# Optimization experiments

Hardware: AMD Instinct MI355X
Metric: run time of the kernel (lower is better)

Reference implementation:

```python
import jax, jax.numpy as jnp
import numpy as np

N_DIMS, N_EMBD, N_LAYER = 64, 256, 12
B, N = 32, 1024
LN_EPS = 1e-5


def setup_inputs() -> dict:
    key = jax.random.key(0)
    ks = jax.random.split(key, 16)
    s = 0.02
    inp = {
        'xs': jax.random.normal(ks[0], (B, N, N_DIMS - 1), dtype=jnp.float32),
        'ys': jax.random.normal(ks[1], (B, N), dtype=jnp.float32),
        # read-in linear
        'W_in': jax.random.normal(ks[2], (N_DIMS, N_EMBD), dtype=jnp.float32) * s,
        'b_in': jnp.zeros((N_EMBD,), jnp.float32),
        # per-layer attention projections (no bias)
        'Wq': jax.random.normal(ks[3], (N_LAYER, N_EMBD, N_EMBD), dtype=jnp.float32) * s,
        'Wk': jax.random.normal(ks[4], (N_LAYER, N_EMBD, N_EMBD), dtype=jnp.float32) * s,
        'Wv': jax.random.normal(ks[5], (N_LAYER, N_EMBD, N_EMBD), dtype=jnp.float32) * s,
        # layernorm 1
        'g1': jnp.ones((N_LAYER, N_EMBD), jnp.float32),
        'be1': jnp.zeros((N_LAYER, N_EMBD), jnp.float32),
        # mlp: Linear -> ReLU -> Linear
        'W1': jax.random.normal(ks[6], (N_LAYER, N_EMBD, N_EMBD), dtype=jnp.float32) * s,
        'b1': jnp.zeros((N_LAYER, N_EMBD), jnp.float32),
        'W2': jax.random.normal(ks[7], (N_LAYER, N_EMBD, N_EMBD), dtype=jnp.float32) * s,
        'b2': jnp.zeros((N_LAYER, N_EMBD), jnp.float32),
        # layernorm 2
        'g2': jnp.ones((N_LAYER, N_EMBD), jnp.float32),
        'be2': jnp.zeros((N_LAYER, N_EMBD), jnp.float32),
        # read-out linear
        'W_out': jax.random.normal(ks[8], (N_EMBD, 1), dtype=jnp.float32) * s,
        'b_out': jnp.zeros((1,), jnp.float32),
    }
    return inp


def _layernorm(x, g, b):
    mu = jnp.mean(x, axis=-1, keepdims=True)
    var = jnp.mean(jnp.square(x - mu), axis=-1, keepdims=True)
    return (x - mu) * jax.lax.rsqrt(var + LN_EPS) * g + b


def reference(xs, ys, W_in, b_in, Wq, Wk, Wv, g1, be1, W1, b1, W2, b2, g2, be2, W_out, b_out):
    n = ys.shape[1]
    # _combine: zs [B, N, d+1], zero the y slot of the last (test) token
    zs = jnp.concatenate([xs, ys[:, :, None]], axis=2)
    zs = zs.at[:, -1, -1].set(0.0)
    H = zs @ W_in + b_in  # [B, N, E]
    for i in range(N_LAYER):
        q = H @ Wq[i]
        k = H @ Wk[i]
        v = H @ Wv[i]
        attn = jax.nn.relu(jnp.einsum('bid,bjd->bij', q, k)) / n
        H = H + jnp.einsum('bij,bjd->bid', attn, v)
        H = _layernorm(H, g1[i], be1[i])
        H = H + (jax.nn.relu(H @ W1[i] + b1[i]) @ W2[i] + b2[i])
        H = _layernorm(H, g2[i], be2[i])
    pred = H @ W_out + b_out  # [B, N, 1]
    return pred[:, :n, 0]  # default inds = arange(ys.shape[1])
```

## Files before the change

kernel.cpp:

```cpp
#include <hip/hip_runtime.h>
#include <math.h>

#define E 256
#define NTOK 1024
#define NB 32
#define NLAYER 12
#define LN_EPS 1e-5f

typedef __attribute__((ext_vector_type(8))) short bf16x8;
typedef __attribute__((ext_vector_type(4))) float f32x4;
#define MFMA16(a, b, c) __builtin_amdgcn_mfma_f32_16x16x32_bf16(a, b, c, 0, 0, 0)

__device__ __forceinline__ ushort f2bf(float f) {
    union { float f; unsigned u; } v; v.f = f;
    return (ushort)((v.u + 0x7fffu + ((v.u >> 16) & 1u)) >> 16);
}

__global__ __launch_bounds__(256) void k_wprep(
    const float* __restrict__ Wq, const float* __restrict__ Wk, const float* __restrict__ Wv,
    const float* __restrict__ W1, const float* __restrict__ W2,
    ushort* __restrict__ WT)
{
    const int mat = blockIdx.x % 5;
    const int l   = blockIdx.x / 5;
    const float* src = (mat == 0 ? Wq : mat == 1 ? Wk : mat == 2 ? Wv : mat == 3 ? W1 : W2)
                       + (size_t)l * E * E;
    ushort* dst = WT + ((size_t)(l * 5 + mat) << 16);
    const int n = threadIdx.x;
    #pragma unroll
    for (int c = 0; c < 4; ++c) {
        #pragma unroll
        for (int j = 0; j < 8; ++j) {
            const int k0 = c * 64 + j * 8;
            uint4 u;
            u.x = (uint)f2bf(src[(size_t)(k0 + 0) * E + n]) | ((uint)f2bf(src[(size_t)(k0 + 1) * E + n]) << 16);
            u.y = (uint)f2bf(src[(size_t)(k0 + 2) * E + n]) | ((uint)f2bf(src[(size_t)(k0 + 3) * E + n]) << 16);
            u.z = (uint)f2bf(src[(size_t)(k0 + 4) * E + n]) | ((uint)f2bf(src[(size_t)(k0 + 5) * E + n]) << 16);
            u.w = (uint)f2bf(src[(size_t)(k0 + 6) * E + n]) | ((uint)f2bf(src[(size_t)(k0 + 7) * E + n]) << 16);
            *(uint4*)&dst[(size_t)n * E + k0] = u;
        }
    }
}

__global__ __launch_bounds__(256) void k_embed(
    const float* __restrict__ xs, const float* __restrict__ ys,
    const float* __restrict__ W_in, const float* __restrict__ b_in,
    float* __restrict__ H, ushort* __restrict__ Hb)
{
    __shared__ float zs[16][64];
    const int tid = threadIdx.x;
    const int r0 = blockIdx.x * 16;
    #pragma unroll
    for (int l = 0; l < 4; ++l) {
        int lin = tid + l * 256;
        int i = lin >> 6, d = lin & 63;
        int row = r0 + i;
        int t = row & (NTOK - 1);
        float v;
        if (d < 63) v = xs[(size_t)row * 63 + d];
        else        v = (t == NTOK - 1) ? 0.f : ys[row];
        zs[i][d] = v;
    }
    __syncthreads();
    float acc[16];
    #pragma unroll
    for (int i = 0; i < 16; ++i) acc[i] = 0.f;
    for (int d = 0; d < 64; ++d) {
        float w = W_in[d * E + tid];
        #pragma unroll
        for (int i = 0; i < 16; ++i) acc[i] = fmaf(zs[i][d], w, acc[i]);
    }
    float bb = b_in[tid];
    #pragma unroll
    for (int i = 0; i < 16; ++i) {
        float o = acc[i] + bb;
        H [(size_t)(r0 + i) * E + tid] = o;
        Hb[(size_t)(r0 + i) * E + tid] = f2bf(o);
    }
}

__device__ __forceinline__ void qkv_gemm(
    const ushort* __restrict__ Wt, const ushort* __restrict__ Hb,
    size_t r0, int tid, int w, int lr, int lg,
    ushort (&Ws)[256][72], f32x4 (&acc)[4][4])
{
    #pragma unroll
    for (int mt = 0; mt < 4; ++mt)
        #pragma unroll
        for (int nt = 0; nt < 4; ++nt) acc[mt][nt] = (f32x4){0.f, 0.f, 0.f, 0.f};
    #pragma unroll 1
    for (int kc = 0; kc < 4; ++kc) {
        __syncthreads();
        #pragma unroll
        for (int rep = 0; rep < 8; ++rep) {
            int lin = rep * 256 + tid;
            int n = lin >> 3, slot = lin & 7;
            bf16x8 v = *(const bf16x8*)&Wt[(size_t)n * E + kc * 64 + slot * 8];
            *(bf16x8*)&Ws[n][slot * 8] = v;
        }
        __syncthreads();
        #pragma unroll
        for (int kl = 0; kl < 2; ++kl) {
            bf16x8 af[4], bw[4];
            #pragma unroll
            for (int mt = 0; mt < 4; ++mt)
                af[mt] = *(const bf16x8*)&Hb[(r0 + mt * 16 + lr) * E + kc * 64 + kl * 32 + lg * 8];
            #pragma unroll
            for (int nt = 0; nt < 4; ++nt)
                bw[nt] = *(const bf16x8*)&Ws[w * 64 + nt * 16 + lr][kl * 32 + lg * 8];
            #pragma unroll
            for (int mt = 0; mt < 4; ++mt)
                #pragma unroll
                for (int nt = 0; nt < 4; ++nt)
                    acc[mt][nt] = MFMA16(af[mt], bw[nt], acc[mt][nt]);
        }
    }
}

__device__ __forceinline__ void qkv_out_qk(
    ushort* __restrict__ Out, size_t r0, int w, int l, int lr, int lg,
    ushort (&ScW)[16][72], f32x4 (&acc)[4][4])
{
    #pragma unroll
    for (int mt = 0; mt < 4; ++mt) {
        #pragma unroll
        for (int nt = 0; nt < 4; ++nt)
            #pragma unroll
            for (int r = 0; r < 4; ++r)
                ScW[lg * 4 + r][nt * 16 + lr] = f2bf(acc[mt][nt][r]);
        #pragma unroll
        for (int j = 0; j < 2; ++j) {
            bf16x8 v = *(const bf16x8*)&ScW[l >> 2][(l & 3) * 16 + j * 8];
            *(bf16x8*)&Out[(r0 + mt * 16 + (l >> 2)) * E + w * 64 + (l & 3) * 16 + j * 8] = v;
        }
    }
}

__global__ __launch_bounds__(256, 2) void k_qkv(
    const ushort* __restrict__ Hb,
    const ushort* __restrict__ WqT, const ushort* __restrict__ WkT, const ushort* __restrict__ WvT,
    ushort* __restrict__ Qb, ushort* __restrict__ Kb, ushort* __restrict__ VTg)
{
    __shared__ __align__(16) ushort Ws[256][72];
    __shared__ __align__(16) ushort Sc[4][16][72];
    const int tid = threadIdx.x;
    const int w = tid >> 6, l = tid & 63;
    const int lr = l & 15, lg = l >> 4;
    const size_t r0 = (size_t)blockIdx.x * 64;
    const int b    = (int)(r0 >> 10);
    const int tok0 = (int)(r0 & (NTOK - 1));

    f32x4 acc[4][4];

    qkv_gemm(WqT, Hb, r0, tid, w, lr, lg, Ws, acc);
    qkv_out_qk(Qb, r0, w, l, lr, lg, Sc[w], acc);

    qkv_gemm(WkT, Hb, r0, tid, w, lr, lg, Ws, acc);
    qkv_out_qk(Kb, r0, w, l, lr, lg, Sc[w], acc);

    qkv_gemm(WvT, Hb, r0, tid, w, lr, lg, Ws, acc);
    __syncthreads();
    #pragma unroll
    for (int mt = 0; mt < 4; ++mt)
        #pragma unroll
        for (int nt = 0; nt < 4; ++nt) {
            ushort4 u;
            u.x = f2bf(acc[mt][nt][0]); u.y = f2bf(acc[mt][nt][1]);
            u.z = f2bf(acc[mt][nt][2]); u.w = f2bf(acc[mt][nt][3]);
            *(ushort4*)&Ws[w * 64 + nt * 16 + lr][mt * 16 + lg * 4] = u;
        }
    __syncthreads();
    #pragma unroll
    for (int rep = 0; rep < 8; ++rep) {
        int lin = rep * 256 + tid;
        int row = lin >> 3, ch = lin & 7;
        bf16x8 v = *(const bf16x8*)&Ws[row][ch * 8];
        *(bf16x8*)&VTg[((size_t)b * E + row) * NTOK + tok0 + ch * 8] = v;
    }
}

__global__ __launch_bounds__(512, 2) void k_attn(
    const ushort* __restrict__ Qb, const ushort* __restrict__ Kb, const ushort* __restrict__ VTg,
    float* __restrict__ H, ushort* __restrict__ HbO,
    const float* __restrict__ g1, const float* __restrict__ be1)
{
    __shared__ __align__(16) ushort Ks[64][264];
    __shared__ __align__(16) ushort VT[256][72];
    __shared__ __align__(16) ushort Pl[8][16][72];
    const int tid = threadIdx.x;
    const int w  = tid >> 6, l = tid & 63;
    const int lr = l & 15, lg = l >> 4;

    const int bid   = blockIdx.x;
    const int batch = bid & 31;
    const int tile  = bid >> 5;

    const size_t kvbase = (size_t)batch * NTOK * E;
    const size_t vtbase = (size_t)batch * E * NTOK;
    const int    qrow0  = tile * 128 + w * 16;
    const size_t qbase  = kvbase + (size_t)qrow0 * E;

    bf16x8 qf[8];
    #pragma unroll
    for (int kk = 0; kk < 8; ++kk)
        qf[kk] = *(const bf16x8*)&Qb[qbase + (size_t)lr * E + kk * 32 + lg * 8];

    f32x4 o[16];
    #pragma unroll
    for (int nt = 0; nt < 16; ++nt) o[nt] = (f32x4){0.f, 0.f, 0.f, 0.f};

    const float inv_n = 1.0f / (float)NTOK;
    const int krow = tid >> 5, kch = tid & 31;
    const int vrow = tid >> 3, vch = tid & 7;

    bf16x8 ck0, ck1, ck2, ck3, cv0, cv1, cv2, cv3;
    {
        ck0 = *(const bf16x8*)&Kb[kvbase + (size_t)( 0 + krow) * E + kch * 8];
        ck1 = *(const bf16x8*)&Kb[kvbase + (size_t)(16 + krow) * E + kch * 8];
        ck2 = *(const bf16x8*)&Kb[kvbase + (size_t)(32 + krow) * E + kch * 8];
        ck3 = *(const bf16x8*)&Kb[kvbase + (size_t)(48 + krow) * E + kch * 8];
        cv0 = *(const bf16x8*)&VTg[vtbase + (size_t)(  0 + vrow) * NTOK + vch * 8];
        cv1 = *(const bf16x8*)&VTg[vtbase + (size_t)( 64 + vrow) * NTOK + vch * 8];
        cv2 = *(const bf16x8*)&VTg[vtbase + (size_t)(128 + vrow) * NTOK + vch * 8];
        cv3 = *(const bf16x8*)&VTg[vtbase + (size_t)(192 + vrow) * NTOK + vch * 8];
    }

    #pragma unroll 1
    for (int jt = 0; jt < 16; ++jt) {
        __syncthreads();
        *(bf16x8*)&Ks[ 0 + krow][kch * 8] = ck0;
        *(bf16x8*)&Ks[16 + krow][kch * 8] = ck1;
        *(bf16x8*)&Ks[32 + krow][kch * 8] = ck2;
        *(bf16x8*)&Ks[48 + krow][kch * 8] = ck3;
        *(bf16x8*)&VT[  0 + vrow][vch * 8] = cv0;
        *(bf16x8*)&VT[ 64 + vrow][vch * 8] = cv1;
        *(bf16x8*)&VT[128 + vrow][vch * 8] = cv2;
        *(bf16x8*)&VT[192 + vrow][vch * 8] = cv3;
        bf16x8 nk0, nk1, nk2, nk3, nv0, nv1, nv2, nv3;
        {
            const int kn = ((jt + 1) & 15) * 64;
            nk0 = *(const bf16x8*)&Kb[kvbase + (size_t)(kn +  0 + krow) * E + kch * 8];
            nk1 = *(const bf16x8*)&Kb[kvbase + (size_t)(kn + 16 + krow) * E + kch * 8];
            nk2 = *(const bf16x8*)&Kb[kvbase + (size_t)(kn + 32 + krow) * E + kch * 8];
            nk3 = *(const bf16x8*)&Kb[kvbase + (size_t)(kn + 48 + krow) * E + kch * 8];
            nv0 = *(const bf16x8*)&VTg[vtbase + (size_t)(  0 + vrow) * NTOK + kn + vch * 8];
            nv1 = *(const bf16x8*)&VTg[vtbase + (size_t)( 64 + vrow) * NTOK + kn + vch * 8];
            nv2 = *(const bf16x8*)&VTg[vtbase + (size_t)(128 + vrow) * NTOK + kn + vch * 8];
            nv3 = *(const bf16x8*)&VTg[vtbase + (size_t)(192 + vrow) * NTOK + kn + vch * 8];
        }
        __syncthreads();

        __builtin_amdgcn_s_setprio(1);
        f32x4 s0 = (f32x4){0.f, 0.f, 0.f, 0.f};
        f32x4 s1 = s0, s2 = s0, s3 = s0;
        #pragma unroll
        for (int kk = 0; kk < 8; ++kk) {
            bf16x8 b0 = *(const bf16x8*)&Ks[     lr][kk * 32 + lg * 8];
            bf16x8 b1 = *(const bf16x8*)&Ks[16 + lr][kk * 32 + lg * 8];
            bf16x8 b2 = *(const bf16x8*)&Ks[32 + lr][kk * 32 + lg * 8];
            bf16x8 b3 = *(const bf16x8*)&Ks[48 + lr][kk * 32 + lg * 8];
            s0 = MFMA16(qf[kk], b0, s0);
            s1 = MFMA16(qf[kk], b1, s1);
            s2 = MFMA16(qf[kk], b2, s2);
            s3 = MFMA16(qf[kk], b3, s3);
        }
        #pragma unroll
        for (int r = 0; r < 4; ++r) {
            Pl[w][lg * 4 + r][     lr] = f2bf(fmaxf(s0[r], 0.f) * inv_n);
            Pl[w][lg * 4 + r][16 + lr] = f2bf(fmaxf(s1[r], 0.f) * inv_n);
            Pl[w][lg * 4 + r][32 + lr] = f2bf(fmaxf(s2[r], 0.f) * inv_n);
            Pl[w][lg * 4 + r][48 + lr] = f2bf(fmaxf(s3[r], 0.f) * inv_n);
        }
        bf16x8 pa0 = *(const bf16x8*)&Pl[w][lr][lg * 8];
        bf16x8 pa1 = *(const bf16x8*)&Pl[w][lr][32 + lg * 8];
        #pragma unroll
        for (int nt = 0; nt < 16; ++nt) {
            bf16x8 vb0 = *(const bf16x8*)&VT[nt * 16 + lr][lg * 8];
            bf16x8 vb1 = *(const bf16x8*)&VT[nt * 16 + lr][32 + lg * 8];
            o[nt] = MFMA16(pa0, vb0, o[nt]);
            o[nt] = MFMA16(pa1, vb1, o[nt]);
        }
        __builtin_amdgcn_s_setprio(0);
        ck0 = nk0; ck1 = nk1; ck2 = nk2; ck3 = nk3;
        cv0 = nv0; cv1 = nv1; cv2 = nv2; cv3 = nv3;
    }

    float gg[16], bb[16];
    #pragma unroll
    for (int nt = 0; nt < 16; ++nt) {
        gg[nt] = g1[nt * 16 + lr];
        bb[nt] = be1[nt * 16 + lr];
    }
    #pragma unroll
    for (int r = 0; r < 4; ++r) {
        const int q = lg * 4 + r;
        const size_t rowbase = kvbase + (size_t)(qrow0 + q) * E;
        float xv[16];
        float s = 0.f, s2 = 0.f;
        #pragma unroll
        for (int nt = 0; nt < 16; ++nt) {
            float val = H[rowbase + nt * 16 + lr] + o[nt][r];
            xv[nt] = val;
            s += val; s2 += val * val;
        }
        #pragma unroll
        for (int m = 1; m < 16; m <<= 1) {
            s  += __shfl_xor(s, m, 64);
            s2 += __shfl_xor(s2, m, 64);
        }
        float mu = s * (1.f / 256.f);
        float rs = rsqrtf(s2 * (1.f / 256.f) - mu * mu + LN_EPS);
        #pragma unroll
        for (int nt = 0; nt < 16; ++nt) {
            float ov = (xv[nt] - mu) * rs * gg[nt] + bb[nt];
            H  [rowbase + nt * 16 + lr] = ov;
            HbO[rowbase + nt * 16 + lr] = f2bf(ov);
        }
    }
}

__global__ __launch_bounds__(256, 2) void k_mlp(
    const ushort* __restrict__ Hb, float* __restrict__ H, ushort* __restrict__ HbO,
    const ushort* __restrict__ W1T, const float* __restrict__ b1,
    const ushort* __restrict__ W2T, const float* __restrict__ b2,
    const float* __restrict__ g2, const float* __restrict__ be2)
{
    __shared__ __align__(16) ushort Ws[256][72];
    __shared__ __align__(16) ushort Ts[64][264];
    __shared__ float part[4][64][2];
    __shared__ float stats[64][2];
    const int tid = threadIdx.x;
    const int w = tid >> 6, l = tid & 63;
    const int lr = l & 15, lg = l >> 4;
    const size_t r0 = (size_t)blockIdx.x * 64;

    f32x4 acc[4][4];
    qkv_gemm(W1T, Hb, r0, tid, w, lr, lg, Ws, acc);
    {
        float bb1[4];
        #pragma unroll
        for (int nt = 0; nt < 4; ++nt) bb1[nt] = b1[w * 64 + nt * 16 + lr];
        #pragma unroll
        for (int mt = 0; mt < 4; ++mt)
            #pragma unroll
            for (int nt = 0; nt < 4; ++nt)
                #pragma unroll
                for (int r = 0; r < 4; ++r)
                    Ts[mt * 16 + lg * 4 + r][w * 64 + nt * 16 + lr]
                        = f2bf(fmaxf(acc[mt][nt][r] + bb1[nt], 0.f));
    }

    f32x4 acc2[4][4];
    #pragma unroll
    for (int mt = 0; mt < 4; ++mt)
        #pragma unroll
        for (int nt = 0; nt < 4; ++nt) acc2[mt][nt] = (f32x4){0.f, 0.f, 0.f, 0.f};
    #pragma unroll 1
    for (int kc = 0; kc < 4; ++kc) {
        __syncthreads();
        #pragma unroll
        for (int rep = 0; rep < 8; ++rep) {
            int lin = rep * 256 + tid;
            int n = lin >> 3, slot = lin & 7;
            bf16x8 v = *(const bf16x8*)&W2T[(size_t)n * E + kc * 64 + slot * 8];
            *(bf16x8*)&Ws[n][slot * 8] = v;
        }
        __syncthreads();
        #pragma unroll
        for (int kl = 0; kl < 2; ++kl) {
            bf16x8 af[4], bw[4];
            #pragma unroll
            for (int mt = 0; mt < 4; ++mt)
                af[mt] = *(const bf16x8*)&Ts[mt * 16 + lr][kc * 64 + kl * 32 + lg * 8];
            #pragma unroll
            for (int nt = 0; nt < 4; ++nt)
                bw[nt] = *(const bf16x8*)&Ws[w * 64 + nt * 16 + lr][kl * 32 + lg * 8];
            #pragma unroll
            for (int mt = 0; mt < 4; ++mt)
                #pragma unroll
                for (int nt = 0; nt < 4; ++nt)
                    acc2[mt][nt] = MFMA16(af[mt], bw[nt], acc2[mt][nt]);
        }
    }

    {
        float b2v[4];
        #pragma unroll
        for (int nt = 0; nt < 4; ++nt) b2v[nt] = b2[w * 64 + nt * 16 + lr];
        #pragma unroll
        for (int mt = 0; mt < 4; ++mt)
            #pragma unroll
            for (int r = 0; r < 4; ++r)
                #pragma unroll
                for (int nt = 0; nt < 4; ++nt)
                    acc2[mt][nt][r] += H[(r0 + mt * 16 + lg * 4 + r) * E + w * 64 + nt * 16 + lr]
                                       + b2v[nt];
    }
    #pragma unroll
    for (int mt = 0; mt < 4; ++mt)
        #pragma unroll
        for (int r = 0; r < 4; ++r) {
            float s = 0.f, s2 = 0.f;
            #pragma unroll
            for (int nt = 0; nt < 4; ++nt) {
                float v = acc2[mt][nt][r];
                s += v; s2 += v * v;
            }
            #pragma unroll
            for (int m = 1; m < 16; m <<= 1) {
                s  += __shfl_xor(s, m, 64);
                s2 += __shfl_xor(s2, m, 64);
            }
            if (lr == 0) {
                part[w][mt * 16 + lg * 4 + r][0] = s;
                part[w][mt * 16 + lg * 4 + r][1] = s2;
            }
        }
    __syncthreads();
    if (tid < 64) {
        float s = part[0][tid][0] + part[1][tid][0] + part[2][tid][0] + part[3][tid][0];
        float s2 = part[0][tid][1] + part[1][tid][1] + part[2][tid][1] + part[3][tid][1];
        float mu = s * (1.f / 256.f);
        stats[tid][0] = mu;
        stats[tid][1] = rsqrtf(s2 * (1.f / 256.f) - mu * mu + LN_EPS);
    }
    __syncthreads();
    {
        float gg[4], be[4];
        #pragma unroll
        for (int nt = 0; nt < 4; ++nt) {
            gg[nt] = g2[w * 64 + nt * 16 + lr];
            be[nt] = be2[w * 64 + nt * 16 + lr];
        }
        #pragma unroll
        for (int mt = 0; mt < 4; ++mt)
            #pragma unroll
            for (int r = 0; r < 4; ++r) {
                const int row = mt * 16 + lg * 4 + r;
                const float mu = stats[row][0], rs = stats[row][1];
                const size_t rowbase = (r0 + row) * E;
                #pragma unroll
                for (int nt = 0; nt < 4; ++nt) {
                    float ov = (acc2[mt][nt][r] - mu) * rs * gg[nt] + be[nt];
                    H  [rowbase + w * 64 + nt * 16 + lr] = ov;
                    HbO[rowbase + w * 64 + nt * 16 + lr] = f2bf(ov);
                }
            }
    }
}

__global__ __launch_bounds__(256) void k_readout(
    const float* __restrict__ H, const float* __restrict__ W_out,
    const float* __restrict__ b_out, float* __restrict__ out)
{
    const int tid = threadIdx.x;
    const int lane = tid & 63;
    const int row = blockIdx.x * 4 + (tid >> 6);
    float s = 0.f;
    #pragma unroll
    for (int j = 0; j < 4; ++j)
        s += H[(size_t)row * E + j * 64 + lane] * W_out[j * 64 + lane];
    #pragma unroll
    for (int m = 1; m < 64; m <<= 1) s += __shfl_xor(s, m, 64);
    if (lane == 0) out[row] = s + b_out[0];
}

extern "C" void kernel_launch(void* const* d_in, const int* in_sizes, int n_in,
                              void* d_out, int out_size, void* d_ws, size_t ws_size,
                              hipStream_t stream)
{
    const float* xs    = (const float*)d_in[0];
    const float* ys    = (const float*)d_in[1];
    const float* W_in  = (const float*)d_in[2];
    const float* b_in  = (const float*)d_in[3];
    const float* Wq    = (const float*)d_in[4];
    const float* Wk    = (const float*)d_in[5];
    const float* Wv    = (const float*)d_in[6];
    const float* g1    = (const float*)d_in[7];
    const float* be1   = (const float*)d_in[8];
    const float* W1    = (const float*)d_in[9];
    const float* b1    = (const float*)d_in[10];
    const float* W2    = (const float*)d_in[11];
    const float* b2    = (const float*)d_in[12];
    const float* g2    = (const float*)d_in[13];
    const float* be2   = (const float*)d_in[14];
    const float* W_out = (const float*)d_in[15];
    const float* b_out = (const float*)d_in[16];
    (void)in_sizes; (void)n_in; (void)out_size; (void)ws_size;

    const size_t SZ = (size_t)NB * NTOK * E;
    float*  H   = (float*)d_ws;
    ushort* Hb  = (ushort*)(H + SZ);
    ushort* Qb  = Hb + SZ;
    ushort* Kb  = Qb + SZ;
    ushort* VTg = Kb + SZ;
    ushort* WT  = VTg + SZ;

    k_wprep<<<dim3(NLAYER * 5), dim3(256), 0, stream>>>(Wq, Wk, Wv, W1, W2, WT);
    k_embed<<<dim3(2048), dim3(256), 0, stream>>>(xs, ys, W_in, b_in, H, Hb);
    for (int i = 0; i < NLAYER; ++i) {
        const size_t vo = (size_t)i * E;
        const ushort* WqT = WT + ((size_t)(i * 5 + 0) << 16);
        const ushort* WkT = WT + ((size_t)(i * 5 + 1) << 16);
        const ushort* WvT = WT + ((size_t)(i * 5 + 2) << 16);
        const ushort* W1T = WT + ((size_t)(i * 5 + 3) << 16);
        const ushort* W2T = WT + ((size_t)(i * 5 + 4) << 16);
        k_qkv<<<dim3(512), dim3(256), 0, stream>>>(Hb, WqT, WkT, WvT, Qb, Kb, VTg);
        k_attn<<<dim3(256), dim3(512), 0, stream>>>(Qb, Kb, VTg, H, Hb, g1 + vo, be1 + vo);
        k_mlp<<<dim3(512), dim3(256), 0, stream>>>(Hb, H, Hb, W1T, b1 + vo, W2T, b2 + vo,
                                                   g2 + vo, be2 + vo);
    }
    k_readout<<<dim3((NB * NTOK) / 4), dim3(256), 0, stream>>>(H, W_out, b_out, (float*)d_out);
}
```

Baseline: 1.749 ms.

## Switch attention kernel to 32x32x16 MFMA with 32-row waves and smaller KV tiles

Reworks the attention kernel to use 32x32x16 bf16 MFMA instead of 16x16x32. Each wave now owns 32 query rows, with 4 waves per block instead of 8, and K/V are staged in 32-token tiles over 32 iterations. The layernorm epilogue is remapped to the 32x32 accumulator layout. Fewer, larger MFMAs give more work per LDS fragment load, but the block size drops to 256 threads, and with launch bounds of 1 per SIMD and larger accumulators per thread, occupancy and latency hiding may fall.

```diff
diff --git a/kernel.cpp b/kernel.cpp
--- a/kernel.cpp
+++ b/kernel.cpp
@@ -9,7 +9,9 @@
 
 typedef __attribute__((ext_vector_type(8))) short bf16x8;
 typedef __attribute__((ext_vector_type(4))) float f32x4;
+typedef __attribute__((ext_vector_type(16))) float f32x16;
 #define MFMA16(a, b, c) __builtin_amdgcn_mfma_f32_16x16x32_bf16(a, b, c, 0, 0, 0)
+#define MFMA32(a, b, c) __builtin_amdgcn_mfma_f32_32x32x16_bf16(a, b, c, 0, 0, 0)
 
 __device__ __forceinline__ ushort f2bf(float f) {
     union { float f; unsigned u; } v; v.f = f;
@@ -179,17 +181,18 @@
     }
 }
 
-__global__ __launch_bounds__(512, 2) void k_attn(
+__global__ __launch_bounds__(256, 1) void k_attn(
     const ushort* __restrict__ Qb, const ushort* __restrict__ Kb, const ushort* __restrict__ VTg,
     float* __restrict__ H, ushort* __restrict__ HbO,
     const float* __restrict__ g1, const float* __restrict__ be1)
 {
-    __shared__ __align__(16) ushort Ks[64][264];
-    __shared__ __align__(16) ushort VT[256][72];
-    __shared__ __align__(16) ushort Pl[8][16][72];
+    __shared__ __align__(16) ushort Ks[32][264];
+    __shared__ __align__(16) ushort VT[256][40];
+    __shared__ __align__(16) ushort Pl[4][32][40];
     const int tid = threadIdx.x;
     const int w  = tid >> 6, l = tid & 63;
-    const int lr = l & 15, lg = l >> 4;
+    const int lq = l & 31;
+    const int h  = l >> 5;
 
     const int bid   = blockIdx.x;
     const int batch = bid & 31;
@@ -197,28 +200,30 @@
 
     const size_t kvbase = (size_t)batch * NTOK * E;
     const size_t vtbase = (size_t)batch * E * NTOK;
-    const int    qrow0  = tile * 128 + w * 16;
+    const int    qrow0  = tile * 128 + w * 32;
     const size_t qbase  = kvbase + (size_t)qrow0 * E;
 
-    bf16x8 qf[8];
-    #pragma unroll
-    for (int kk = 0; kk < 8; ++kk)
-        qf[kk] = *(const bf16x8*)&Qb[qbase + (size_t)lr * E + kk * 32 + lg * 8];
-
-    f32x4 o[16];
-    #pragma unroll
-    for (int nt = 0; nt < 16; ++nt) o[nt] = (f32x4){0.f, 0.f, 0.f, 0.f};
+    bf16x8 qf[16];
+    #pragma unroll
+    for (int ks = 0; ks < 16; ++ks)
+        qf[ks] = *(const bf16x8*)&Qb[qbase + (size_t)lq * E + ks * 16 + h * 8];
+
+    f32x16 o[8];
+    #pragma unroll
+    for (int et = 0; et < 8; ++et)
+        #pragma unroll
+        for (int j = 0; j < 16; ++j) o[et][j] = 0.f;
 
     const float inv_n = 1.0f / (float)NTOK;
     const int krow = tid >> 5, kch = tid & 31;
-    const int vrow = tid >> 3, vch = tid & 7;
+    const int vrow = tid >> 2, vch = tid & 3;
 
     bf16x8 ck0, ck1, ck2, ck3, cv0, cv1, cv2, cv3;
     {
         ck0 = *(const bf16x8*)&Kb[kvbase + (size_t)( 0 + krow) * E + kch * 8];
-        ck1 = *(const bf16x8*)&Kb[kvbase + (size_t)(16 + krow) * E + kch * 8];
-        ck2 = *(const bf16x8*)&Kb[kvbase + (size_t)(32 + krow) * E + kch * 8];
-        ck3 = *(const bf16x8*)&Kb[kvbase + (size_t)(48 + krow) * E + kch * 8];
+        ck1 = *(const bf16x8*)&Kb[kvbase + (size_t)( 8 + krow) * E + kch * 8];
+        ck2 = *(const bf16x8*)&Kb[kvbase + (size_t)(16 + krow) * E + kch * 8];
+        ck3 = *(const bf16x8*)&Kb[kvbase + (size_t)(24 + krow) * E + kch * 8];
         cv0 = *(const bf16x8*)&VTg[vtbase + (size_t)(  0 + vrow) * NTOK + vch * 8];
         cv1 = *(const bf16x8*)&VTg[vtbase + (size_t)( 64 + vrow) * NTOK + vch * 8];
         cv2 = *(const bf16x8*)&VTg[vtbase + (size_t)(128 + vrow) * NTOK + vch * 8];
@@ -226,23 +231,23 @@
     }
 
     #pragma unroll 1
-    for (int jt = 0; jt < 16; ++jt) {
+    for (int jt = 0; jt < 32; ++jt) {
         __syncthreads();
         *(bf16x8*)&Ks[ 0 + krow][kch * 8] = ck0;
-        *(bf16x8*)&Ks[16 + krow][kch * 8] = ck1;
-        *(bf16x8*)&Ks[32 + krow][kch * 8] = ck2;
-        *(bf16x8*)&Ks[48 + krow][kch * 8] = ck3;
+        *(bf16x8*)&Ks[ 8 + krow][kch * 8] = ck1;
+        *(bf16x8*)&Ks[16 + krow][kch * 8] = ck2;
+        *(bf16x8*)&Ks[24 + krow][kch * 8] = ck3;
         *(bf16x8*)&VT[  0 + vrow][vch * 8] = cv0;
         *(bf16x8*)&VT[ 64 + vrow][vch * 8] = cv1;
         *(bf16x8*)&VT[128 + vrow][vch * 8] = cv2;
         *(bf16x8*)&VT[192 + vrow][vch * 8] = cv3;
         bf16x8 nk0, nk1, nk2, nk3, nv0, nv1, nv2, nv3;
         {
-            const int kn = ((jt + 1) & 15) * 64;
+            const int kn = ((jt + 1) & 31) * 32;
             nk0 = *(const bf16x8*)&Kb[kvbase + (size_t)(kn +  0 + krow) * E + kch * 8];
-            nk1 = *(const bf16x8*)&Kb[kvbase + (size_t)(kn + 16 + krow) * E + kch * 8];
-            nk2 = *(const bf16x8*)&Kb[kvbase + (size_t)(kn + 32 + krow) * E + kch * 8];
-            nk3 = *(const bf16x8*)&Kb[kvbase + (size_t)(kn + 48 + krow) * E + kch * 8];
+            nk1 = *(const bf16x8*)&Kb[kvbase + (size_t)(kn +  8 + krow) * E + kch * 8];
+            nk2 = *(const bf16x8*)&Kb[kvbase + (size_t)(kn + 16 + krow) * E + kch * 8];
+            nk3 = *(const bf16x8*)&Kb[kvbase + (size_t)(kn + 24 + krow) * E + kch * 8];
             nv0 = *(const bf16x8*)&VTg[vtbase + (size_t)(  0 + vrow) * NTOK + kn + vch * 8];
             nv1 = *(const bf16x8*)&VTg[vtbase + (size_t)( 64 + vrow) * NTOK + kn + vch * 8];
             nv2 = *(const bf16x8*)&VTg[vtbase + (size_t)(128 + vrow) * NTOK + kn + vch * 8];
@@ -251,70 +256,61 @@
         __syncthreads();
 
         __builtin_amdgcn_s_setprio(1);
-        f32x4 s0 = (f32x4){0.f, 0.f, 0.f, 0.f};
-        f32x4 s1 = s0, s2 = s0, s3 = s0;
-        #pragma unroll
-        for (int kk = 0; kk < 8; ++kk) {
-            bf16x8 b0 = *(const bf16x8*)&Ks[     lr][kk * 32 + lg * 8];
-            bf16x8 b1 = *(const bf16x8*)&Ks[16 + lr][kk * 32 + lg * 8];
-            bf16x8 b2 = *(const bf16x8*)&Ks[32 + lr][kk * 32 + lg * 8];
-            bf16x8 b3 = *(const bf16x8*)&Ks[48 + lr][kk * 32 + lg * 8];
-            s0 = MFMA16(qf[kk], b0, s0);
-            s1 = MFMA16(qf[kk], b1, s1);
-            s2 = MFMA16(qf[kk], b2, s2);
-            s3 = MFMA16(qf[kk], b3, s3);
-        }
-        #pragma unroll
-        for (int r = 0; r < 4; ++r) {
-            Pl[w][lg * 4 + r][     lr] = f2bf(fmaxf(s0[r], 0.f) * inv_n);
-            Pl[w][lg * 4 + r][16 + lr] = f2bf(fmaxf(s1[r], 0.f) * inv_n);
-            Pl[w][lg * 4 + r][32 + lr] = f2bf(fmaxf(s2[r], 0.f) * inv_n);
-            Pl[w][lg * 4 + r][48 + lr] = f2bf(fmaxf(s3[r], 0.f) * inv_n);
-        }
-        bf16x8 pa0 = *(const bf16x8*)&Pl[w][lr][lg * 8];
-        bf16x8 pa1 = *(const bf16x8*)&Pl[w][lr][32 + lg * 8];
-        #pragma unroll
-        for (int nt = 0; nt < 16; ++nt) {
-            bf16x8 vb0 = *(const bf16x8*)&VT[nt * 16 + lr][lg * 8];
-            bf16x8 vb1 = *(const bf16x8*)&VT[nt * 16 + lr][32 + lg * 8];
-            o[nt] = MFMA16(pa0, vb0, o[nt]);
-            o[nt] = MFMA16(pa1, vb1, o[nt]);
+        f32x16 s;
+        #pragma unroll
+        for (int j = 0; j < 16; ++j) s[j] = 0.f;
+        #pragma unroll
+        for (int ks = 0; ks < 16; ++ks) {
+            bf16x8 kb = *(const bf16x8*)&Ks[lq][ks * 16 + h * 8];
+            s = MFMA32(qf[ks], kb, s);
+        }
+        #pragma unroll
+        for (int r = 0; r < 16; ++r)
+            Pl[w][(r & 3) + 8 * (r >> 2) + 4 * h][lq] = f2bf(fmaxf(s[r], 0.f) * inv_n);
+        bf16x8 pa0 = *(const bf16x8*)&Pl[w][lq][h * 8];
+        bf16x8 pa1 = *(const bf16x8*)&Pl[w][lq][16 + h * 8];
+        #pragma unroll
+        for (int et = 0; et < 8; ++et) {
+            bf16x8 vb0 = *(const bf16x8*)&VT[et * 32 + lq][h * 8];
+            bf16x8 vb1 = *(const bf16x8*)&VT[et * 32 + lq][16 + h * 8];
+            o[et] = MFMA32(pa0, vb0, o[et]);
+            o[et] = MFMA32(pa1, vb1, o[et]);
         }
         __builtin_amdgcn_s_setprio(0);
         ck0 = nk0; ck1 = nk1; ck2 = nk2; ck3 = nk3;
         cv0 = nv0; cv1 = nv1; cv2 = nv2; cv3 = nv3;
     }
 
-    float gg[16], bb[16];
-    #pragma unroll
-    for (int nt = 0; nt < 16; ++nt) {
-        gg[nt] = g1[nt * 16 + lr];
-        bb[nt] = be1[nt * 16 + lr];
-    }
-    #pragma unroll
-    for (int r = 0; r < 4; ++r) {
-        const int q = lg * 4 + r;
-        const size_t rowbase = kvbase + (size_t)(qrow0 + q) * E;
-        float xv[16];
+    float gg[8], bb[8];
+    #pragma unroll
+    for (int et = 0; et < 8; ++et) {
+        gg[et] = g1[et * 32 + lq];
+        bb[et] = be1[et * 32 + lq];
+    }
+    #pragma unroll
+    for (int r = 0; r < 16; ++r) {
+        const int qloc = (r & 3) + 8 * (r >> 2) + 4 * h;
+        const size_t rowbase = kvbase + (size_t)(qrow0 + qloc) * E;
+        float xv[8];
         float s = 0.f, s2 = 0.f;
         #pragma unroll
-        for (int nt = 0; nt < 16; ++nt) {
-            float val = H[rowbase + nt * 16 + lr] + o[nt][r];
-            xv[nt] = val;
+        for (int et = 0; et < 8; ++et) {
+            float val = H[rowbase + et * 32 + lq] + o[et][r];
+            xv[et] = val;
             s += val; s2 += val * val;
         }
         #pragma unroll
-        for (int m = 1; m < 16; m <<= 1) {
+        for (int m = 1; m < 32; m <<= 1) {
             s  += __shfl_xor(s, m, 64);
             s2 += __shfl_xor(s2, m, 64);
         }
         float mu = s * (1.f / 256.f);
         float rs = rsqrtf(s2 * (1.f / 256.f) - mu * mu + LN_EPS);
         #pragma unroll
-        for (int nt = 0; nt < 16; ++nt) {
-            float ov = (xv[nt] - mu) * rs * gg[nt] + bb[nt];
-            H  [rowbase + nt * 16 + lr] = ov;
-            HbO[rowbase + nt * 16 + lr] = f2bf(ov);
+        for (int et = 0; et < 8; ++et) {
+            float ov = (xv[et] - mu) * rs * gg[et] + bb[et];
+            H  [rowbase + et * 32 + lq] = ov;
+            HbO[rowbase + et * 32 + lq] = f2bf(ov);
         }
     }
 }
@@ -506,7 +502,7 @@
         const ushort* W1T = WT + ((size_t)(i * 5 + 3) << 16);
         const ushort* W2T = WT + ((size_t)(i * 5 + 4) << 16);
         k_qkv<<<dim3(512), dim3(256), 0, stream>>>(Hb, WqT, WkT, WvT, Qb, Kb, VTg);
-        k_attn<<<dim3(256), dim3(512), 0, stream>>>(Qb, Kb, VTg, H, Hb, g1 + vo, be1 + vo);
+        k_attn<<<dim3(256), dim3(256), 0, stream>>>(Qb, Kb, VTg, H, Hb, g1 + vo, be1 + vo);
         k_mlp<<<dim3(512), dim3(256), 0, stream>>>(Hb, H, Hb, W1T, b1 + vo, W2T, b2 + vo,
                                                    g2 + vo, be2 + vo);
     }
```

After: 1.795 ms. 2.7% more time.
